# Kernel tuning notes

Hardware: AMD Instinct MI355X
Metric: run time of the kernel (lower is better)

Reference implementation:

```python
import jax, jax.numpy as jnp
import numpy as np

N_EMBD = 1024
HEAD_SIZE = 64
WINDOW_SIZE = 256


def setup_inputs() -> dict:
    key = jax.random.key(0)
    kx, kk, kq, kv = jax.random.split(key, 4)
    B, T = 4, 4096
    x = jax.random.normal(kx, (B, T, N_EMBD), dtype=jnp.float32)
    # Linear(n_embd, head_size, bias=False): y = x @ W where W is [n_embd, head_size]
    scale = 1.0 / np.sqrt(N_EMBD)
    Wk = jax.random.normal(kk, (N_EMBD, HEAD_SIZE), dtype=jnp.float32) * scale
    Wq = jax.random.normal(kq, (N_EMBD, HEAD_SIZE), dtype=jnp.float32) * scale
    Wv = jax.random.normal(kv, (N_EMBD, HEAD_SIZE), dtype=jnp.float32) * scale
    return {"x": x, "Wk": Wk, "Wq": Wq, "Wv": Wv}


def reference(x, Wk, Wq, Wv):
    B, T, C = x.shape
    k = jnp.einsum('btc,ch->bth', x, Wk)  # [B,T,H]
    q = jnp.einsum('btc,ch->bth', x, Wq)
    v = jnp.einsum('btc,ch->bth', x, Wv)
    scale = k.shape[-1] ** -0.5
    weights = jnp.einsum('bqh,bkh->bqk', q, k) * scale  # [B,T,T]
    rows = jnp.arange(T)[:, None]
    cols = jnp.arange(T)[None, :]
    # causal AND within sliding window of WINDOW_SIZE
    mask = (rows >= cols) & (cols >= rows - WINDOW_SIZE + 1)
    weights = jnp.where(mask, weights, -jnp.inf)
    weights = jax.nn.softmax(weights, axis=-1)
    out = jnp.einsum('bqk,bkh->bqh', weights, v)  # [B,T,H]
    return out
```

## Files before the change

kernel.cpp:

```cpp
#include <hip/hip_runtime.h>
#include <float.h>

#define TSEQ 4096
#define CEMB 1024
#define NH 64
#define WIN 256

typedef __attribute__((ext_vector_type(8))) short  s16x8;
typedef __attribute__((ext_vector_type(4))) float  f32x4;
typedef unsigned short ush;

__device__ __forceinline__ void split2(float f, ush& hi, ush& lo) {
    unsigned b = __float_as_uint(f);
    hi = (ush)(b >> 16);
    float hf = __uint_as_float(b & 0xFFFF0000u);
    lo = (ush)(__float_as_uint(f - hf) >> 16);
}

__device__ __forceinline__ void split8(f32x4 a, f32x4 b, s16x8& hi, s16x8& lo) {
    #pragma unroll
    for (int j = 0; j < 4; ++j) { ush h, l; split2(a[j], h, l); hi[j] = (short)h; lo[j] = (short)l; }
    #pragma unroll
    for (int j = 0; j < 4; ++j) { ush h, l; split2(b[j], h, l); hi[4+j] = (short)h; lo[4+j] = (short)l; }
}

#define MFMA(a, b, c) __builtin_amdgcn_mfma_f32_16x16x32_bf16((a), (b), (c), 0, 0, 0)

__global__ __launch_bounds__(256)
void w_convert(const float* __restrict__ Wk, const float* __restrict__ Wq,
               const float* __restrict__ Wv,
               ush* __restrict__ Wth, ush* __restrict__ Wtl)
{
    const int m  = blockIdx.x >> 4;
    const int k0 = (blockIdx.x & 15) << 6;
    const float* src = (m == 0) ? Wk : ((m == 1) ? Wq : Wv);
    #pragma unroll
    for (int i = 0; i < 16; ++i) {
        const int idx = threadIdx.x + (i << 8);
        const int r = idx >> 6, c = idx & 63;
        const float v = src[(k0 + r) * NH + c];
        ush h, l; split2(v, h, l);
        const int o = (m * 64 + c) * CEMB + k0 + r;
        Wth[o] = h; Wtl[o] = l;
    }
}

__device__ __forceinline__ int swz(int row, int chunk) {
    return row * 32 + (((chunk) ^ ((row >> 1) & 3)) << 3);
}

__global__ __launch_bounds__(256)
void qkv_proj(const float* __restrict__ x,
              const ush* __restrict__ Wth, const ush* __restrict__ Wtl,
              ush* __restrict__ kbh, ush* __restrict__ kbl,
              ush* __restrict__ qbh, ush* __restrict__ qbl,
              ush* __restrict__ vbh, ush* __restrict__ vbl)
{
    __shared__ short Ah[2][32 * 32], Al[2][32 * 32];
    __shared__ short Bh[2][192 * 32], Bl[2][192 * 32];

    const int tid = threadIdx.x;
    const int m0  = blockIdx.x << 5;
    const int w   = tid >> 6;
    const int l15 = tid & 15;
    const int g   = (tid >> 4) & 3;

    const bool aact = tid < 128;
    const int arow  = tid >> 2;
    const int ach   = tid & 3;
    const float* xp = x + (size_t)(m0 + (aact ? arow : 0)) * CEMB + (ach << 3);

    int wn[3], wch[3];
    #pragma unroll
    for (int i = 0; i < 3; ++i) {
        const int c = tid + (i << 8);
        wn[i] = c >> 2; wch[i] = c & 3;
    }

    f32x4 acc[2][3];
    #pragma unroll
    for (int i = 0; i < 2; ++i)
        #pragma unroll
        for (int j = 0; j < 3; ++j) acc[i][j] = (f32x4){0.f, 0.f, 0.f, 0.f};

    f32x4 xr0 = {0,0,0,0}, xr1 = {0,0,0,0};
    if (aact) { xr0 = *(const f32x4*)(xp); xr1 = *(const f32x4*)(xp + 4); }
    s16x8 wrh[3], wrl[3];
    #pragma unroll
    for (int i = 0; i < 3; ++i) {
        const int o = wn[i] * CEMB + (wch[i] << 3);
        wrh[i] = *(const s16x8*)&Wth[o];
        wrl[i] = *(const s16x8*)&Wtl[o];
    }

    for (int t = 0; t < 32; ++t) {
        const int cur = t & 1;
        if (aact) {
            s16x8 vh, vl; split8(xr0, xr1, vh, vl);
            const int ao = swz(arow, ach);
            *(s16x8*)&Ah[cur][ao] = vh;
            *(s16x8*)&Al[cur][ao] = vl;
        }
        #pragma unroll
        for (int i = 0; i < 3; ++i) {
            const int bo = swz(wn[i], wch[i]);
            *(s16x8*)&Bh[cur][bo] = wrh[i];
            *(s16x8*)&Bl[cur][bo] = wrl[i];
        }
        __syncthreads();
        if (t < 31) {
            const int k0 = (t + 1) << 5;
            if (aact) { xr0 = *(const f32x4*)(xp + k0); xr1 = *(const f32x4*)(xp + k0 + 4); }
            #pragma unroll
            for (int i = 0; i < 3; ++i) {
                const int o = wn[i] * CEMB + k0 + (wch[i] << 3);
                wrh[i] = *(const s16x8*)&Wth[o];
                wrl[i] = *(const s16x8*)&Wtl[o];
            }
        }
        s16x8 afh[2], afl[2], bfh[3], bfl[3];
        #pragma unroll
        for (int rt = 0; rt < 2; ++rt) {
            const int o = swz(rt * 16 + l15, g);
            afh[rt] = *(const s16x8*)&Ah[cur][o];
            afl[rt] = *(const s16x8*)&Al[cur][o];
        }
        #pragma unroll
        for (int ct = 0; ct < 3; ++ct) {
            const int o = swz(w * 48 + ct * 16 + l15, g);
            bfh[ct] = *(const s16x8*)&Bh[cur][o];
            bfl[ct] = *(const s16x8*)&Bl[cur][o];
        }
        #pragma unroll
        for (int rt = 0; rt < 2; ++rt)
            #pragma unroll
            for (int ct = 0; ct < 3; ++ct) {
                acc[rt][ct] = MFMA(afh[rt], bfh[ct], acc[rt][ct]);
                acc[rt][ct] = MFMA(afh[rt], bfl[ct], acc[rt][ct]);
                acc[rt][ct] = MFMA(afl[rt], bfh[ct], acc[rt][ct]);
            }
    }

    #pragma unroll
    for (int ct = 0; ct < 3; ++ct) {
        const int colbase = w * 48 + ct * 16;
        ush* oph; ush* opl;
        if (colbase < 64)       { oph = kbh; opl = kbl; }
        else if (colbase < 128) { oph = qbh; opl = qbl; }
        else                    { oph = vbh; opl = vbl; }
        const int col = (colbase & 63) + l15;
        #pragma unroll
        for (int rt = 0; rt < 2; ++rt)
            #pragma unroll
            for (int r = 0; r < 4; ++r) {
                const size_t row = m0 + rt * 16 + g * 4 + r;
                ush h, l; split2(acc[rt][ct][r], h, l);
                oph[row * NH + col] = h;
                opl[row * NH + col] = l;
            }
    }
}

__global__ __launch_bounds__(256)
void v_transpose(const ush* __restrict__ vbh, const ush* __restrict__ vbl,
                 ush* __restrict__ vbTh, ush* __restrict__ vbTl)
{
    const int k0  = blockIdx.x << 6;
    const int b   = blockIdx.y;
    const int dim = threadIdx.x & 63;
    const int j16 = threadIdx.x >> 6;
    const size_t inb = ((size_t)b * TSEQ + k0 + j16 * 16) * NH + dim;
    s16x8 h0, h1, l0, l1;
    #pragma unroll
    for (int j = 0; j < 8; ++j) {
        h0[j] = (short)vbh[inb + (size_t)j * NH];
        l0[j] = (short)vbl[inb + (size_t)j * NH];
    }
    #pragma unroll
    for (int j = 0; j < 8; ++j) {
        h1[j] = (short)vbh[inb + (size_t)(8 + j) * NH];
        l1[j] = (short)vbl[inb + (size_t)(8 + j) * NH];
    }
    const size_t ob = (size_t)b * (64 * TSEQ) + (size_t)dim * TSEQ + k0 + j16 * 16;
    *(s16x8*)&vbTh[ob]     = h0;
    *(s16x8*)&vbTh[ob + 8] = h1;
    *(s16x8*)&vbTl[ob]     = l0;
    *(s16x8*)&vbTl[ob + 8] = l1;
}

__global__ __launch_bounds__(256)
void attn_swin(const ush* __restrict__ qbh, const ush* __restrict__ qbl,
               const ush* __restrict__ kbh, const ush* __restrict__ kbl,
               const ush* __restrict__ vbTh, const ush* __restrict__ vbTl,
               float* __restrict__ out)
{
    __shared__ ush Ph[4][16 * 64], Pl[4][16 * 64];
    __shared__ float cO[4][16][68];
    __shared__ float cm[4][16], cl[4][16];

    const int tid = threadIdx.x;
    const int w   = tid >> 6;
    const int l15 = tid & 15;
    const int g   = (tid >> 4) & 3;
    const int u   = l15 & 7;
    const int q0  = blockIdx.x << 4;
    const int b   = blockIdx.y;
    const size_t tbase = (size_t)b * TSEQ;
    const size_t vtb   = (size_t)b * (64 * TSEQ);

    const int qrow = q0 + l15;

    s16x8 Qh[2], Ql[2];
    #pragma unroll
    for (int ks = 0; ks < 2; ++ks) {
        const size_t o = (tbase + qrow) * NH + ks * 32 + g * 8;
        Qh[ks] = *(const s16x8*)&qbh[o];
        Ql[ks] = *(const s16x8*)&qbl[o];
    }

    f32x4 O[4];
    #pragma unroll
    for (int i = 0; i < 4; ++i) O[i] = (f32x4){0.f, 0.f, 0.f, 0.f};
    float m_run = -FLT_MAX, l_run = 0.f;

    int lo = q0 - (WIN - 1); if (lo < 0) lo = 0;
    const int t_lo = lo >> 6, t_hi = q0 >> 6;

    for (int t = t_lo + w; t <= t_hi; t += 4) {
        const int k0 = t << 6;

        f32x4 S[4];
        #pragma unroll
        for (int kt = 0; kt < 4; ++kt) {
            f32x4 s = (f32x4){0.f, 0.f, 0.f, 0.f};
            #pragma unroll
            for (int ks = 0; ks < 2; ++ks) {
                const size_t o = (tbase + k0 + kt * 16 + l15) * NH + ks * 32 + g * 8;
                s16x8 kh = *(const s16x8*)&kbh[o];
                s16x8 kl = *(const s16x8*)&kbl[o];
                s = MFMA(kh, Qh[ks], s);
                s = MFMA(kh, Ql[ks], s);
                s = MFMA(kl, Qh[ks], s);
            }
            S[kt] = s;
        }

        float mt = -FLT_MAX;
        #pragma unroll
        for (int kt = 0; kt < 4; ++kt)
            #pragma unroll
            for (int r = 0; r < 4; ++r) {
                const int key = k0 + kt * 16 + g * 4 + r;
                const float s = S[kt][r] * 0.125f;
                S[kt][r] = s;
                if ((key <= qrow) && (key > qrow - WIN)) mt = fmaxf(mt, s);
            }
        mt = fmaxf(mt, __shfl_xor(mt, 16));
        mt = fmaxf(mt, __shfl_xor(mt, 32));
        const float mn  = fmaxf(m_run, mt);
        const float fsc = __expf(m_run - mn);

        float sum = 0.f;
        #pragma unroll
        for (int kt = 0; kt < 4; ++kt) {
            const int chunk = kt * 2 + (g >> 1);
            const int c2 = (chunk + u) & 7;
            const int abase = l15 * 64 + c2 * 8 + (g & 1) * 4;
            #pragma unroll
            for (int rp = 0; rp < 4; rp += 2) {
                const int key0 = k0 + kt * 16 + g * 4 + rp;
                const bool v0 = (key0     <= qrow) && (key0     > qrow - WIN);
                const bool v1 = (key0 + 1 <= qrow) && (key0 + 1 > qrow - WIN);
                const float p0 = v0 ? __expf(S[kt][rp]     - mn) : 0.f;
                const float p1 = v1 ? __expf(S[kt][rp + 1] - mn) : 0.f;
                sum += p0 + p1;
                ush h0, lo0, h1, lo1;
                split2(p0, h0, lo0); split2(p1, h1, lo1);
                *(unsigned int*)&Ph[w][abase + rp] = (unsigned int)h0  | ((unsigned int)h1  << 16);
                *(unsigned int*)&Pl[w][abase + rp] = (unsigned int)lo0 | ((unsigned int)lo1 << 16);
            }
        }
        sum += __shfl_xor(sum, 16);
        sum += __shfl_xor(sum, 32);
        l_run = l_run * fsc + sum;
        m_run = mn;

        float fr[4];
        #pragma unroll
        for (int r = 0; r < 4; ++r) fr[r] = __shfl(fsc, g * 4 + r);
        #pragma unroll
        for (int dt = 0; dt < 4; ++dt)
            #pragma unroll
            for (int r = 0; r < 4; ++r) O[dt][r] *= fr[r];

        #pragma unroll
        for (int ks = 0; ks < 2; ++ks) {
            const int c2r = ((ks * 4 + g) + u) & 7;
            const int po = l15 * 64 + c2r * 8;
            s16x8 pah = *(const s16x8*)&Ph[w][po];
            s16x8 pal = *(const s16x8*)&Pl[w][po];
            #pragma unroll
            for (int dt = 0; dt < 4; ++dt) {
                const size_t vo = vtb + (size_t)(dt * 16 + l15) * TSEQ + k0 + ks * 32 + g * 8;
                s16x8 vh = *(const s16x8*)&vbTh[vo];
                s16x8 vl = *(const s16x8*)&vbTl[vo];
                O[dt] = MFMA(pah, vh, O[dt]);
                O[dt] = MFMA(pah, vl, O[dt]);
                O[dt] = MFMA(pal, vh, O[dt]);
            }
        }
    }

    if (g == 0) { cm[w][l15] = m_run; cl[w][l15] = l_run; }
    #pragma unroll
    for (int dt = 0; dt < 4; ++dt)
        #pragma unroll
        for (int r = 0; r < 4; ++r)
            cO[w][g * 4 + r][dt * 16 + l15] = O[dt][r];
    __syncthreads();

    {
        const int dt = w;
        #pragma unroll
        for (int r = 0; r < 4; ++r) {
            const int row = g * 4 + r;
            const float mm0 = cm[0][row], mm1 = cm[1][row], mm2 = cm[2][row], mm3 = cm[3][row];
            const float ms = fmaxf(fmaxf(mm0, mm1), fmaxf(mm2, mm3));
            const float f0 = __expf(mm0 - ms), f1 = __expf(mm1 - ms);
            const float f2 = __expf(mm2 - ms), f3 = __expf(mm3 - ms);
            const float ll = f0 * cl[0][row] + f1 * cl[1][row] + f2 * cl[2][row] + f3 * cl[3][row];
            const int col = dt * 16 + l15;
            const float oo = f0 * cO[0][row][col] + f1 * cO[1][row][col]
                           + f2 * cO[2][row][col] + f3 * cO[3][row][col];
            out[(tbase + q0 + row) * NH + col] = oo / ll;
        }
    }
}

extern "C" void kernel_launch(void* const* d_in, const int* in_sizes, int n_in,
                              void* d_out, int out_size, void* d_ws, size_t ws_size,
                              hipStream_t stream)
{
    const float* x  = (const float*)d_in[0];
    const float* Wk = (const float*)d_in[1];
    const float* Wq = (const float*)d_in[2];
    const float* Wv = (const float*)d_in[3];
    float* out = (float*)d_out;

    const int Bn = in_sizes[0] / (TSEQ * CEMB);
    const size_t perBuf = (size_t)Bn * TSEQ * NH;

    ush* base = (ush*)d_ws;
    ush* kbh = base;
    ush* kbl = kbh + perBuf;
    ush* qbh = kbl + perBuf;
    ush* qbl = qbh + perBuf;
    ush* vbh = qbl + perBuf;
    ush* vbl = vbh + perBuf;
    ush* vbTh = vbl + perBuf;
    ush* vbTl = vbTh + perBuf;
    ush* Wth = vbTl + perBuf;
    ush* Wtl = Wth + 192 * CEMB;

    w_convert<<<dim3(48), dim3(256), 0, stream>>>(Wk, Wq, Wv, Wth, Wtl);
    qkv_proj<<<dim3((Bn * TSEQ) / 32), dim3(256), 0, stream>>>(x, Wth, Wtl,
                                                               kbh, kbl, qbh, qbl, vbh, vbl);
    v_transpose<<<dim3(TSEQ / 64, Bn), dim3(256), 0, stream>>>(vbh, vbl, vbTh, vbTl);
    attn_swin<<<dim3(TSEQ / 16, Bn), dim3(256), 0, stream>>>(qbh, qbl, kbh, kbl,
                                                             vbTh, vbTl, out);
}
```

Measured before the change: 173.2 us.

## Restructure all kernels: LDS-staged transposes, direct-to-LDS x loads, shared K/V tiles

The weight conversion and V transpose now stage through LDS so global writes are coalesced 16-byte vectors. The QKV projection uses global_load_lds to pull fp32 x straight into swizzled LDS, widens the K step to 64 and splits into bf16 hi/lo at fragment-load time. The attention kernel now gives each block 64 queries (one 16-row tile per wave), so the four waves share K and V tiles in LDS instead of splitting keys across waves, and the cross-wave softmax merge is removed. MFMA sections are wrapped in s_setprio. In exchange there are more barriers per tile and each wave covers the whole window serially.

```diff
diff --git a/kernel.cpp b/kernel.cpp
--- a/kernel.cpp
+++ b/kernel.cpp
@@ -26,27 +26,42 @@
 
 #define MFMA(a, b, c) __builtin_amdgcn_mfma_f32_16x16x32_bf16((a), (b), (c), 0, 0, 0)
 
+__device__ __forceinline__ void load_lds16(const void* g, void* l) {
+    __builtin_amdgcn_global_load_lds(
+        (const __attribute__((address_space(1))) unsigned int*)g,
+        (__attribute__((address_space(3))) unsigned int*)l, 16, 0, 0);
+}
+
 __global__ __launch_bounds__(256)
 void w_convert(const float* __restrict__ Wk, const float* __restrict__ Wq,
                const float* __restrict__ Wv,
                ush* __restrict__ Wth, ush* __restrict__ Wtl)
 {
+    __shared__ ush Lh[64][66], Ll[64][66];
     const int m  = blockIdx.x >> 4;
     const int k0 = (blockIdx.x & 15) << 6;
     const float* src = (m == 0) ? Wk : ((m == 1) ? Wq : Wv);
-    #pragma unroll
-    for (int i = 0; i < 16; ++i) {
-        const int idx = threadIdx.x + (i << 8);
-        const int r = idx >> 6, c = idx & 63;
-        const float v = src[(k0 + r) * NH + c];
-        ush h, l; split2(v, h, l);
-        const int o = (m * 64 + c) * CEMB + k0 + r;
-        Wth[o] = h; Wtl[o] = l;
-    }
-}
-
-__device__ __forceinline__ int swz(int row, int chunk) {
-    return row * 32 + (((chunk) ^ ((row >> 1) & 3)) << 3);
+
+    const int kr = threadIdx.x >> 2;
+    const int cq = threadIdx.x & 3;
+    #pragma unroll
+    for (int j = 0; j < 4; ++j) {
+        const f32x4 v = *(const f32x4*)&src[(k0 + kr) * NH + cq * 16 + j * 4];
+        #pragma unroll
+        for (int e = 0; e < 4; ++e) {
+            ush h, l; split2(v[e], h, l);
+            const int c = cq * 16 + j * 4 + e;
+            Lh[c][kr] = h; Ll[c][kr] = l;
+        }
+    }
+    __syncthreads();
+    const int n  = threadIdx.x >> 2;
+    const int kc = threadIdx.x & 3;
+    const size_t ob = (size_t)(m * 64 + n) * CEMB + k0 + kc * 16;
+    *(s16x8*)&Wth[ob]     = *(const s16x8*)&Lh[n][kc * 16];
+    *(s16x8*)&Wth[ob + 8] = *(const s16x8*)&Lh[n][kc * 16 + 8];
+    *(s16x8*)&Wtl[ob]     = *(const s16x8*)&Ll[n][kc * 16];
+    *(s16x8*)&Wtl[ob + 8] = *(const s16x8*)&Ll[n][kc * 16 + 8];
 }
 
 __global__ __launch_bounds__(256)
@@ -56,25 +71,31 @@
               ush* __restrict__ qbh, ush* __restrict__ qbl,
               ush* __restrict__ vbh, ush* __restrict__ vbl)
 {
-    __shared__ short Ah[2][32 * 32], Al[2][32 * 32];
-    __shared__ short Bh[2][192 * 32], Bl[2][192 * 32];
+    __shared__ float Axs[2][32 * 64];
+    __shared__ ush  Bh[192 * 64], Bl[192 * 64];
 
     const int tid = threadIdx.x;
     const int m0  = blockIdx.x << 5;
     const int w   = tid >> 6;
+    const int ln  = tid & 63;
     const int l15 = tid & 15;
     const int g   = (tid >> 4) & 3;
 
-    const bool aact = tid < 128;
-    const int arow  = tid >> 2;
-    const int ach   = tid & 3;
-    const float* xp = x + (size_t)(m0 + (aact ? arow : 0)) * CEMB + (ach << 3);
-
-    int wn[3], wch[3];
-    #pragma unroll
-    for (int i = 0; i < 3; ++i) {
-        const int c = tid + (i << 8);
-        wn[i] = c >> 2; wch[i] = c & 3;
+    int dmr[2], dmc[2], dmbase[2];
+    #pragma unroll
+    for (int i = 0; i < 2; ++i) {
+        const int d0 = w * 128 + i * 64;
+        const int d  = d0 + ln;
+        dmr[i] = d >> 4;
+        dmc[i] = (d & 15) ^ (dmr[i] & 15);
+        dmbase[i] = d0 * 4;
+    }
+
+    int bn[6], bc[6];
+    #pragma unroll
+    for (int i = 0; i < 6; ++i) {
+        const int s = tid + (i << 8);
+        bn[i] = s >> 3; bc[i] = s & 7;
     }
 
     f32x4 acc[2][3];
@@ -83,68 +104,76 @@
         #pragma unroll
         for (int j = 0; j < 3; ++j) acc[i][j] = (f32x4){0.f, 0.f, 0.f, 0.f};
 
-    f32x4 xr0 = {0,0,0,0}, xr1 = {0,0,0,0};
-    if (aact) { xr0 = *(const f32x4*)(xp); xr1 = *(const f32x4*)(xp + 4); }
-    s16x8 wrh[3], wrl[3];
-    #pragma unroll
-    for (int i = 0; i < 3; ++i) {
-        const int o = wn[i] * CEMB + (wch[i] << 3);
+    #pragma unroll
+    for (int i = 0; i < 2; ++i)
+        load_lds16(&x[(size_t)(m0 + dmr[i]) * CEMB + dmc[i] * 4], &Axs[0][dmbase[i]]);
+    s16x8 wrh[6], wrl[6];
+    #pragma unroll
+    for (int i = 0; i < 6; ++i) {
+        const size_t o = (size_t)bn[i] * CEMB + bc[i] * 8;
         wrh[i] = *(const s16x8*)&Wth[o];
         wrl[i] = *(const s16x8*)&Wtl[o];
     }
 
-    for (int t = 0; t < 32; ++t) {
+    for (int t = 0; t < 16; ++t) {
         const int cur = t & 1;
-        if (aact) {
-            s16x8 vh, vl; split8(xr0, xr1, vh, vl);
-            const int ao = swz(arow, ach);
-            *(s16x8*)&Ah[cur][ao] = vh;
-            *(s16x8*)&Al[cur][ao] = vl;
-        }
-        #pragma unroll
-        for (int i = 0; i < 3; ++i) {
-            const int bo = swz(wn[i], wch[i]);
-            *(s16x8*)&Bh[cur][bo] = wrh[i];
-            *(s16x8*)&Bl[cur][bo] = wrl[i];
+        #pragma unroll
+        for (int i = 0; i < 6; ++i) {
+            const int o = bn[i] * 64 + ((bc[i] ^ (bn[i] & 7)) << 3);
+            *(s16x8*)&Bh[o] = wrh[i];
+            *(s16x8*)&Bl[o] = wrl[i];
         }
         __syncthreads();
-        if (t < 31) {
-            const int k0 = (t + 1) << 5;
-            if (aact) { xr0 = *(const f32x4*)(xp + k0); xr1 = *(const f32x4*)(xp + k0 + 4); }
-            #pragma unroll
-            for (int i = 0; i < 3; ++i) {
-                const int o = wn[i] * CEMB + k0 + (wch[i] << 3);
+
+        if (t < 15) {
+            #pragma unroll
+            for (int i = 0; i < 2; ++i)
+                load_lds16(&x[(size_t)(m0 + dmr[i]) * CEMB + (t + 1) * 64 + dmc[i] * 4],
+                           &Axs[cur ^ 1][dmbase[i]]);
+            #pragma unroll
+            for (int i = 0; i < 6; ++i) {
+                const size_t o = (size_t)bn[i] * CEMB + (t + 1) * 64 + bc[i] * 8;
                 wrh[i] = *(const s16x8*)&Wth[o];
                 wrl[i] = *(const s16x8*)&Wtl[o];
             }
         }
-        s16x8 afh[2], afl[2], bfh[3], bfl[3];
-        #pragma unroll
-        for (int rt = 0; rt < 2; ++rt) {
-            const int o = swz(rt * 16 + l15, g);
-            afh[rt] = *(const s16x8*)&Ah[cur][o];
-            afl[rt] = *(const s16x8*)&Al[cur][o];
-        }
-        #pragma unroll
-        for (int ct = 0; ct < 3; ++ct) {
-            const int o = swz(w * 48 + ct * 16 + l15, g);
-            bfh[ct] = *(const s16x8*)&Bh[cur][o];
-            bfl[ct] = *(const s16x8*)&Bl[cur][o];
-        }
-        #pragma unroll
-        for (int rt = 0; rt < 2; ++rt)
+
+        #pragma unroll
+        for (int ks = 0; ks < 2; ++ks) {
+            s16x8 afh[2], afl[2], bfh[3], bfl[3];
+            #pragma unroll
+            for (int rt = 0; rt < 2; ++rt) {
+                const int row = rt * 16 + l15;
+                const int c0 = ks * 8 + g * 2;
+                const f32x4 a0 = *(const f32x4*)&Axs[cur][row * 64 + ((c0     ^ l15) << 2)];
+                const f32x4 a1 = *(const f32x4*)&Axs[cur][row * 64 + (((c0+1) ^ l15) << 2)];
+                split8(a0, a1, afh[rt], afl[rt]);
+            }
             #pragma unroll
             for (int ct = 0; ct < 3; ++ct) {
-                acc[rt][ct] = MFMA(afh[rt], bfh[ct], acc[rt][ct]);
-                acc[rt][ct] = MFMA(afh[rt], bfl[ct], acc[rt][ct]);
-                acc[rt][ct] = MFMA(afl[rt], bfh[ct], acc[rt][ct]);
-            }
+                const int n = w * 48 + ct * 16 + l15;
+                const int o = n * 64 + (((ks * 4 + g) ^ (n & 7)) << 3);
+                bfh[ct] = *(const s16x8*)&Bh[o];
+                bfl[ct] = *(const s16x8*)&Bl[o];
+            }
+            __builtin_amdgcn_s_setprio(1);
+            #pragma unroll
+            for (int rt = 0; rt < 2; ++rt)
+                #pragma unroll
+                for (int ct = 0; ct < 3; ++ct) {
+                    acc[rt][ct] = MFMA(afh[rt], bfh[ct], acc[rt][ct]);
+                    acc[rt][ct] = MFMA(afh[rt], bfl[ct], acc[rt][ct]);
+                    acc[rt][ct] = MFMA(afl[rt], bfh[ct], acc[rt][ct]);
+                }
+            __builtin_amdgcn_s_setprio(0);
+        }
+        __syncthreads();
     }
 
     #pragma unroll
     for (int ct = 0; ct < 3; ++ct) {
         const int colbase = w * 48 + ct * 16;
-        ush* oph; ush* opl;
+        ush *oph, *opl;
         if (colbase < 64)       { oph = kbh; opl = kbl; }
         else if (colbase < 128) { oph = qbh; opl = qbl; }
         else                    { oph = vbh; opl = vbl; }
@@ -165,27 +194,31 @@
 void v_transpose(const ush* __restrict__ vbh, const ush* __restrict__ vbl,
                  ush* __restrict__ vbTh, ush* __restrict__ vbTl)
 {
-    const int k0  = blockIdx.x << 6;
-    const int b   = blockIdx.y;
-    const int dim = threadIdx.x & 63;
-    const int j16 = threadIdx.x >> 6;
-    const size_t inb = ((size_t)b * TSEQ + k0 + j16 * 16) * NH + dim;
-    s16x8 h0, h1, l0, l1;
-    #pragma unroll
-    for (int j = 0; j < 8; ++j) {
-        h0[j] = (short)vbh[inb + (size_t)j * NH];
-        l0[j] = (short)vbl[inb + (size_t)j * NH];
-    }
-    #pragma unroll
-    for (int j = 0; j < 8; ++j) {
-        h1[j] = (short)vbh[inb + (size_t)(8 + j) * NH];
-        l1[j] = (short)vbl[inb + (size_t)(8 + j) * NH];
-    }
-    const size_t ob = (size_t)b * (64 * TSEQ) + (size_t)dim * TSEQ + k0 + j16 * 16;
-    *(s16x8*)&vbTh[ob]     = h0;
-    *(s16x8*)&vbTh[ob + 8] = h1;
-    *(s16x8*)&vbTl[ob]     = l0;
-    *(s16x8*)&vbTl[ob + 8] = l1;
+    __shared__ ush Th[64][72], Tl[64][72];
+    const int k0 = blockIdx.x << 6;
+    const int b  = blockIdx.y;
+    const int key = threadIdx.x >> 2;
+    const int cp  = (threadIdx.x & 3) << 1;
+    #pragma unroll
+    for (int i = 0; i < 2; ++i) {
+        const int c = cp + i;
+        const size_t o = ((size_t)b * TSEQ + k0 + key) * NH + c * 8;
+        const s16x8 h = *(const s16x8*)&vbh[o];
+        const s16x8 l = *(const s16x8*)&vbl[o];
+        #pragma unroll
+        for (int j = 0; j < 8; ++j) {
+            Th[c * 8 + j][key] = (ush)h[j];
+            Tl[c * 8 + j][key] = (ush)l[j];
+        }
+    }
+    __syncthreads();
+    const int dim = threadIdx.x >> 2;
+    const int kc  = threadIdx.x & 3;
+    const size_t ob = ((size_t)b * 64 + dim) * TSEQ + k0 + kc * 16;
+    *(s16x8*)&vbTh[ob]     = *(const s16x8*)&Th[dim][kc * 16];
+    *(s16x8*)&vbTh[ob + 8] = *(const s16x8*)&Th[dim][kc * 16 + 8];
+    *(s16x8*)&vbTl[ob]     = *(const s16x8*)&Tl[dim][kc * 16];
+    *(s16x8*)&vbTl[ob + 8] = *(const s16x8*)&Tl[dim][kc * 16 + 8];
 }
 
 __global__ __launch_bounds__(256)
@@ -194,26 +227,26 @@
                const ush* __restrict__ vbTh, const ush* __restrict__ vbTl,
                float* __restrict__ out)
 {
+    __shared__ ush Kh[64 * 72], Kl[64 * 72];
+    __shared__ ush Vth[64 * 72], Vtl[64 * 72];
     __shared__ ush Ph[4][16 * 64], Pl[4][16 * 64];
-    __shared__ float cO[4][16][68];
-    __shared__ float cm[4][16], cl[4][16];
 
     const int tid = threadIdx.x;
+    const int q0  = blockIdx.x << 6;
+    const int b   = blockIdx.y;
+    const size_t tb  = (size_t)b * TSEQ;
+    const size_t vtb = (size_t)b * 64;
     const int w   = tid >> 6;
     const int l15 = tid & 15;
     const int g   = (tid >> 4) & 3;
     const int u   = l15 & 7;
-    const int q0  = blockIdx.x << 4;
-    const int b   = blockIdx.y;
-    const size_t tbase = (size_t)b * TSEQ;
-    const size_t vtb   = (size_t)b * (64 * TSEQ);
-
-    const int qrow = q0 + l15;
+
+    const int qrow = q0 + w * 16 + l15;
 
     s16x8 Qh[2], Ql[2];
     #pragma unroll
     for (int ks = 0; ks < 2; ++ks) {
-        const size_t o = (tbase + qrow) * NH + ks * 32 + g * 8;
+        const size_t o = (tb + qrow) * NH + ks * 32 + g * 8;
         Qh[ks] = *(const s16x8*)&qbh[o];
         Ql[ks] = *(const s16x8*)&qbl[o];
     }
@@ -226,24 +259,41 @@
     int lo = q0 - (WIN - 1); if (lo < 0) lo = 0;
     const int t_lo = lo >> 6, t_hi = q0 >> 6;
 
-    for (int t = t_lo + w; t <= t_hi; t += 4) {
+    const int skey = tid >> 2;
+    const int scp  = (tid & 3) << 1;
+
+    for (int t = t_lo; t <= t_hi; ++t) {
         const int k0 = t << 6;
+        __syncthreads();
+        #pragma unroll
+        for (int i = 0; i < 2; ++i) {
+            const int c = scp + i;
+            const size_t ko = (tb + k0 + skey) * NH + c * 8;
+            const size_t vo = (vtb + skey) * TSEQ + k0 + c * 8;
+            *(s16x8*)&Kh[skey * 72 + c * 8]  = *(const s16x8*)&kbh[ko];
+            *(s16x8*)&Kl[skey * 72 + c * 8]  = *(const s16x8*)&kbl[ko];
+            *(s16x8*)&Vth[skey * 72 + c * 8] = *(const s16x8*)&vbTh[vo];
+            *(s16x8*)&Vtl[skey * 72 + c * 8] = *(const s16x8*)&vbTl[vo];
+        }
+        __syncthreads();
 
         f32x4 S[4];
+        __builtin_amdgcn_s_setprio(1);
         #pragma unroll
         for (int kt = 0; kt < 4; ++kt) {
             f32x4 s = (f32x4){0.f, 0.f, 0.f, 0.f};
             #pragma unroll
             for (int ks = 0; ks < 2; ++ks) {
-                const size_t o = (tbase + k0 + kt * 16 + l15) * NH + ks * 32 + g * 8;
-                s16x8 kh = *(const s16x8*)&kbh[o];
-                s16x8 kl = *(const s16x8*)&kbl[o];
-                s = MFMA(kh, Qh[ks], s);
-                s = MFMA(kh, Ql[ks], s);
-                s = MFMA(kl, Qh[ks], s);
+                const int o = (kt * 16 + l15) * 72 + ks * 32 + g * 8;
+                const s16x8 kah = *(const s16x8*)&Kh[o];
+                const s16x8 kal = *(const s16x8*)&Kl[o];
+                s = MFMA(kah, Qh[ks], s);
+                s = MFMA(kah, Ql[ks], s);
+                s = MFMA(kal, Qh[ks], s);
             }
             S[kt] = s;
         }
+        __builtin_amdgcn_s_setprio(0);
 
         float mt = -FLT_MAX;
         #pragma unroll
@@ -263,8 +313,7 @@
         float sum = 0.f;
         #pragma unroll
         for (int kt = 0; kt < 4; ++kt) {
-            const int chunk = kt * 2 + (g >> 1);
-            const int c2 = (chunk + u) & 7;
+            const int c2 = ((kt * 2 + (g >> 1)) + u) & 7;
             const int abase = l15 * 64 + c2 * 8 + (g & 1) * 4;
             #pragma unroll
             for (int rp = 0; rp < 4; rp += 2) {
@@ -295,46 +344,34 @@
 
         #pragma unroll
         for (int ks = 0; ks < 2; ++ks) {
-            const int c2r = ((ks * 4 + g) + u) & 7;
-            const int po = l15 * 64 + c2r * 8;
-            s16x8 pah = *(const s16x8*)&Ph[w][po];
-            s16x8 pal = *(const s16x8*)&Pl[w][po];
+            const int po = l15 * 64 + ((((ks * 4 + g)) + u) & 7) * 8;
+            const s16x8 pah = *(const s16x8*)&Ph[w][po];
+            const s16x8 pal = *(const s16x8*)&Pl[w][po];
+            __builtin_amdgcn_s_setprio(1);
             #pragma unroll
             for (int dt = 0; dt < 4; ++dt) {
-                const size_t vo = vtb + (size_t)(dt * 16 + l15) * TSEQ + k0 + ks * 32 + g * 8;
-                s16x8 vh = *(const s16x8*)&vbTh[vo];
-                s16x8 vl = *(const s16x8*)&vbTl[vo];
-                O[dt] = MFMA(pah, vh, O[dt]);
-                O[dt] = MFMA(pah, vl, O[dt]);
-                O[dt] = MFMA(pal, vh, O[dt]);
-            }
-        }
-    }
-
-    if (g == 0) { cm[w][l15] = m_run; cl[w][l15] = l_run; }
+                const int vo = (dt * 16 + l15) * 72 + ks * 32 + g * 8;
+                const s16x8 vbh8 = *(const s16x8*)&Vth[vo];
+                const s16x8 vbl8 = *(const s16x8*)&Vtl[vo];
+                O[dt] = MFMA(pah, vbh8, O[dt]);
+                O[dt] = MFMA(pah, vbl8, O[dt]);
+                O[dt] = MFMA(pal, vbh8, O[dt]);
+            }
+            __builtin_amdgcn_s_setprio(0);
+        }
+    }
+
+    const float linv = 1.f / l_run;
+    float fr[4];
+    #pragma unroll
+    for (int r = 0; r < 4; ++r) fr[r] = __shfl(linv, g * 4 + r);
     #pragma unroll
     for (int dt = 0; dt < 4; ++dt)
         #pragma unroll
-        for (int r = 0; r < 4; ++r)
-            cO[w][g * 4 + r][dt * 16 + l15] = O[dt][r];
-    __syncthreads();
-
-    {
-        const int dt = w;
-        #pragma unroll
         for (int r = 0; r < 4; ++r) {
-            const int row = g * 4 + r;
-            const float mm0 = cm[0][row], mm1 = cm[1][row], mm2 = cm[2][row], mm3 = cm[3][row];
-            const float ms = fmaxf(fmaxf(mm0, mm1), fmaxf(mm2, mm3));
-            const float f0 = __expf(mm0 - ms), f1 = __expf(mm1 - ms);
-            const float f2 = __expf(mm2 - ms), f3 = __expf(mm3 - ms);
-            const float ll = f0 * cl[0][row] + f1 * cl[1][row] + f2 * cl[2][row] + f3 * cl[3][row];
-            const int col = dt * 16 + l15;
-            const float oo = f0 * cO[0][row][col] + f1 * cO[1][row][col]
-                           + f2 * cO[2][row][col] + f3 * cO[3][row][col];
-            out[(tbase + q0 + row) * NH + col] = oo / ll;
-        }
-    }
+            const int row = q0 + w * 16 + g * 4 + r;
+            out[(tb + row) * NH + dt * 16 + l15] = O[dt][r] * fr[r];
+        }
 }
 
 extern "C" void kernel_launch(void* const* d_in, const int* in_sizes, int n_in,
@@ -366,6 +403,6 @@
     qkv_proj<<<dim3((Bn * TSEQ) / 32), dim3(256), 0, stream>>>(x, Wth, Wtl,
                                                                kbh, kbl, qbh, qbl, vbh, vbl);
     v_transpose<<<dim3(TSEQ / 64, Bn), dim3(256), 0, stream>>>(vbh, vbl, vbTh, vbTl);
-    attn_swin<<<dim3(TSEQ / 16, Bn), dim3(256), 0, stream>>>(qbh, qbl, kbh, kbl,
+    attn_swin<<<dim3(TSEQ / 64, Bn), dim3(256), 0, stream>>>(qbh, qbl, kbh, kbl,
                                                              vbTh, vbTl, out);
 }
```

New measurement: 143.8 us. 1.2x faster.
